# Performance work log

Hardware: AMD Instinct MI355X
Metric: run time of the kernel (lower is better)

Reference implementation:

```python
import jax, jax.numpy as jnp
import numpy as np
from jax import lax

T = 128          # max_length
C_EXPLORE = 10.0 # tanh_exploration
NEG_INF = -1e30  # stand-in for -inf (safe under fp32 softmax)


def setup_inputs() -> dict:
    key = jax.random.key(0)
    ks = jax.random.split(key, 19)
    B, S, E, H = 512, 256, 128, 128
    sc = 0.05
    return {
        "decoder_input": jax.random.normal(ks[0], (B, E), jnp.float32),
        "embedded_inputs": jax.random.normal(ks[1], (S, B, E), jnp.float32),
        "h0": jax.random.normal(ks[2], (B, H), jnp.float32),
        "c0": jax.random.normal(ks[3], (B, H), jnp.float32),
        "context": jax.random.normal(ks[4], (S, B, H), jnp.float32),
        "Wi": jax.random.normal(ks[5], (4 * H, E), jnp.float32) * sc,
        "bi": jax.random.normal(ks[6], (4 * H,), jnp.float32) * sc,
        "Wh": jax.random.normal(ks[7], (4 * H, H), jnp.float32) * sc,
        "bh": jax.random.normal(ks[8], (4 * H,), jnp.float32) * sc,
        "Wq_g": jax.random.normal(ks[9], (H, H), jnp.float32) * sc,
        "bq_g": jax.random.normal(ks[10], (H,), jnp.float32) * sc,
        "Wref_g": jax.random.normal(ks[11], (H, H), jnp.float32) * sc,
        "bref_g": jax.random.normal(ks[12], (H,), jnp.float32) * sc,
        "v_g": jax.random.normal(ks[13], (H,), jnp.float32) * sc,
        "Wq_p": jax.random.normal(ks[14], (H, H), jnp.float32) * sc,
        "bq_p": jax.random.normal(ks[15], (H,), jnp.float32) * sc,
        "Wref_p": jax.random.normal(ks[16], (H, H), jnp.float32) * sc,
        "bref_p": jax.random.normal(ks[17], (H,), jnp.float32) * sc,
        "v_p": jax.random.normal(ks[18], (H,), jnp.float32) * sc,
    }


def _apply_mask(logits, mask, prev_idxs, has_prev):
    # torch: maskk[b, prev]=1; maskk[b,0]=0; logits[maskk]=-inf (only if prev_idxs given)
    B = logits.shape[0]
    m2 = mask.at[jnp.arange(B), prev_idxs].set(True).at[:, 0].set(False)
    m2 = jnp.where(has_prev, m2, mask)
    return jnp.where(m2, NEG_INF, logits), m2


def reference(decoder_input, embedded_inputs, h0, c0, context,
              Wi, bi, Wh, bh,
              Wq_g, bq_g, Wref_g, bref_g, v_g,
              Wq_p, bq_p, Wref_p, bref_p, v_p):
    S, B, E = embedded_inputs.shape
    # conv1d(kernel=1) over fixed context: precompute once (identical math each step)
    e_g = jnp.einsum('oh,sbh->bso', Wref_g, context) + bref_g  # [B,S,H]
    e_p = jnp.einsum('oh,sbh->bso', Wref_p, context) + bref_p  # [B,S,H]
    keys = jax.random.split(jax.random.key(42), T)

    def step(carry, key):
        dec_in, hx, cx, mask, prev, has_prev, finished = carry
        # LSTM cell
        gates = dec_in @ Wi.T + bi + hx @ Wh.T + bh  # [B,4H]
        ig, fg, cg, og = jnp.split(gates, 4, axis=1)
        cy = jax.nn.sigmoid(fg) * cx + jax.nn.sigmoid(ig) * jnp.tanh(cg)
        hy = jax.nn.sigmoid(og) * jnp.tanh(cy)
        # glimpse attention (n_glimpses=1, no tanh clip)
        q = hy @ Wq_g.T + bq_g                                   # [B,H]
        u = jnp.einsum('h,bsh->bs', v_g, jnp.tanh(q[:, None, :] + e_g))
        u, mask = _apply_mask(u, mask, prev, has_prev)
        a = jax.nn.softmax(u, axis=-1)                           # [B,S]
        g_l = jnp.einsum('bsh,bs->bh', e_g, a)                   # bmm(ref, probs)
        # pointer attention with tanh exploration
        q = g_l @ Wq_p.T + bq_p
        u = jnp.einsum('h,bsh->bs', v_p, jnp.tanh(q[:, None, :] + e_p))
        logits = C_EXPLORE * jnp.tanh(u)
        logits, mask = _apply_mask(logits, mask, prev, has_prev)
        probs = jax.nn.softmax(logits, axis=-1)
        # categorical sample from probs == categorical over masked logits
        idx = jax.random.categorical(key, logits).astype(jnp.int32)
        idx = idx * finished
        finished = finished * (idx != 0).astype(jnp.int32)
        dec_in_new = embedded_inputs[idx, jnp.arange(B), :]      # [B,E]
        new_carry = (dec_in_new, hy, cy, mask, idx, jnp.array(True), finished)
        return new_carry, (probs, idx)

    carry0 = (decoder_input, h0, c0,
              jnp.zeros((B, S), bool), jnp.zeros((B,), jnp.int32),
              jnp.array(False), jnp.ones((B,), jnp.int32))
    (_, hx, cx, _, _, _, _), (probs, sels) = lax.scan(step, carry0, keys)
    return probs, sels, hx, cx  # probs [T,B,S], sels [T,B]
```

## Files before the change

kernel.cpp:

```cpp
#include <hip/hip_runtime.h>
#include <stdint.h>

#define BB 512
#define SS 256
#define EE 128
#define HH 128
#define TT 128
#define G4 512

#define NEG_INF_F (-1e30f)
#define TINY_F32  1.17549435e-38f

__device__ __forceinline__ uint32_t rotl32(uint32_t v, int r){ return (v<<r)|(v>>(32-r)); }

__device__ __forceinline__ void threefry2x32(uint32_t k0, uint32_t k1,
                                             uint32_t c0, uint32_t c1,
                                             uint32_t* o0, uint32_t* o1){
  uint32_t ks2 = k0 ^ k1 ^ 0x1BD11BDAu;
  uint32_t x0 = c0 + k0;
  uint32_t x1 = c1 + k1;
#define TF_R(rr) { x0 += x1; x1 = rotl32(x1, rr); x1 ^= x0; }
  TF_R(13) TF_R(15) TF_R(26) TF_R(6)
  x0 += k1; x1 += ks2 + 1u;
  TF_R(17) TF_R(29) TF_R(16) TF_R(24)
  x0 += ks2; x1 += k0 + 2u;
  TF_R(13) TF_R(15) TF_R(26) TF_R(6)
  x0 += k0; x1 += k1 + 3u;
  TF_R(17) TF_R(29) TF_R(16) TF_R(24)
  x0 += k1; x1 += ks2 + 4u;
  TF_R(13) TF_R(15) TF_R(26) TF_R(6)
  x0 += ks2; x1 += k0 + 5u;
#undef TF_R
  *o0 = x0; *o1 = x1;
}

__device__ __forceinline__ float xla_tanhf(float x){
#pragma clang fp contract(off)
  float ax = fabsf(x);
  float xc = fminf(fmaxf(x, -9.0f), 9.0f);
  float x2 = xc*xc;
  float num = -2.76076847742355e-16f;
  num = x2*num + 2.00018790482477e-13f;
  num = x2*num + -8.60467152213735e-11f;
  num = x2*num + 5.12229709037114e-08f;
  num = x2*num + 1.48572235717979e-05f;
  num = x2*num + 6.37261928875436e-04f;
  num = x2*num + 4.89352455891786e-03f;
  num = xc*num;
  float den = 1.19825839466702e-06f;
  den = x2*den + 1.18534705686654e-04f;
  den = x2*den + 2.26843463243900e-03f;
  den = x2*den + 4.89352518554385e-03f;
  return (ax < 4e-4f) ? x : (num/den);
}

__device__ __forceinline__ float xla_sigmoidf(float x){
#pragma clang fp contract(off)
  return 0.5f + 0.5f * xla_tanhf(0.5f * x);
}

__device__ __forceinline__ double wave_sum_f64(double v){
  #pragma unroll
  for (int off = 32; off; off >>= 1) v += __shfl_xor(v, off, 64);
  return v;
}

__global__ __launch_bounds__(256) void precompute_e_kernel(
    const float* __restrict__ ctx, const float* __restrict__ W,
    const float* __restrict__ bias, float* __restrict__ e_out)
{
#pragma clang fp contract(off)
  __shared__ float Ct[64][65];
  __shared__ float Wt[128][65];
  const int tid = threadIdx.x;
  const int tx = tid & 31;
  const int ty = tid >> 5;
  const size_t r0 = (size_t)blockIdx.x * 64;

  double acc[8][4];
  #pragma unroll
  for (int i=0;i<8;++i){
    #pragma unroll
    for (int j=0;j<4;++j) acc[i][j]=0.0;
  }

  for (int kc=0; kc<2; ++kc){
    for (int idx = tid; idx < 64*64; idx += 256){
      const int row = idx >> 6, col = idx & 63;
      Ct[row][col] = ctx[(r0 + row)*HH + kc*64 + col];
    }
    for (int idx = tid; idx < 128*64; idx += 256){
      const int row = idx >> 6, col = idx & 63;
      Wt[row][col] = W[row*HH + kc*64 + col];
    }
    __syncthreads();
    #pragma unroll 4
    for (int kk=0; kk<64; ++kk){
      float cv[8], wv[4];
      #pragma unroll
      for (int i=0;i<8;++i) cv[i] = Ct[ty + 8*i][kk];
      #pragma unroll
      for (int j=0;j<4;++j) wv[j] = Wt[tx + 32*j][kk];
      #pragma unroll
      for (int i=0;i<8;++i){
        #pragma unroll
        for (int j=0;j<4;++j) acc[i][j] += (double)cv[i] * (double)wv[j];
      }
    }
    __syncthreads();
  }
  #pragma unroll
  for (int i=0;i<8;++i){
    const size_t r = r0 + ty + 8*i;
    const int s  = (int)(r >> 9);
    const int bb = (int)(r & 511);
    float* dst = e_out + ((size_t)bb*SS + s)*HH;
    #pragma unroll
    for (int j=0;j<4;++j){
      const int c = tx + 32*j;
      dst[c] = (float)acc[i][j] + bias[c];
    }
  }
}

__global__ void transpose_weights_kernel(
    const float* __restrict__ Wi, const float* __restrict__ Wh,
    const float* __restrict__ Wqg, const float* __restrict__ Wqp,
    float* __restrict__ WiT, float* __restrict__ WhT,
    float* __restrict__ WqgT, float* __restrict__ WqpT)
{
  const int i = blockIdx.x * blockDim.x + threadIdx.x;
  if (i < G4*EE){
    const int j = i / EE, e = i % EE;
    WiT[e*G4 + j] = Wi[i];
    WhT[e*G4 + j] = Wh[i];
  }
  if (i < HH*HH){
    const int o = i / HH, h = i % HH;
    WqgT[h*HH + o] = Wqg[i];
    WqpT[h*HH + o] = Wqp[i];
  }
}

__global__ __launch_bounds__(1024, 4) void decode_kernel(
    const float* __restrict__ dec0, const float* __restrict__ h0v, const float* __restrict__ c0v,
    const float* __restrict__ WiT, const float* __restrict__ WhT,
    const float* __restrict__ bi, const float* __restrict__ bh,
    const float* __restrict__ WqgT, const float* __restrict__ bqg, const float* __restrict__ vg,
    const float* __restrict__ WqpT, const float* __restrict__ bqp, const float* __restrict__ vp,
    const float* __restrict__ e_g, const float* __restrict__ e_p,
    const float* __restrict__ emb,
    float* __restrict__ probs_out, float* __restrict__ sels_out,
    float* __restrict__ hx_out, float* __restrict__ cx_out)
{
#pragma clang fp contract(off)
  const int b = blockIdx.x;
  const int tid = threadIdx.x;
  const int lane = tid & 63;
  const int w = tid >> 6;

  __shared__ float  e_s[SS][HH];
  __shared__ double parts8[8][258];
  __shared__ float  u_s[SS];
  __shared__ float  gates_s[G4];
  __shared__ float  dec_s[EE], hy_s[HH], c_s[HH], gl_s[HH];
  __shared__ float  q4_s[4][132];
  __shared__ float  vg4_s[4][132];
  __shared__ float  vp4_s[4][132];
  __shared__ float  bqg_s[HH], bqp_s[HH];
  __shared__ uint32_t keys0_s[TT], keys1_s[TT];
  __shared__ unsigned char mask_s[SS];
  __shared__ float  fred_s[4];
  __shared__ double dred_s[4];
  __shared__ float  amax_v[4];
  __shared__ int    amax_i[4];
  __shared__ int    idx_sh, fin_sh;

  const float* egb = e_g + (size_t)b*SS*HH;
  const float* epb = e_p + (size_t)b*SS*HH;

  if (tid < HH){
    dec_s[tid] = dec0[b*EE + tid];
    hy_s[tid]  = h0v[b*HH + tid];
    c_s[tid]   = c0v[b*HH + tid];
    const float vgv = vg[tid];
    const float vpv = vp[tid];
    #pragma unroll
    for (int c=0;c<4;++c){ vg4_s[c][tid] = vgv; vp4_s[c][tid] = vpv; }
    bqg_s[tid] = bqg[tid];
    bqp_s[tid] = bqp[tid];
  }
  if (tid < SS) mask_s[tid] = 0;
  if (tid < TT){
    uint32_t kk0, kk1;
    threefry2x32(0u, 42u, 0u, (uint32_t)tid, &kk0, &kk1);
    keys0_s[tid] = kk0; keys1_s[tid] = kk1;
  }
  if (tid == 0) fin_sh = 1;
  for (int idx = tid; idx < SS*32; idx += 1024){
    const int r  = idx >> 5;
    const int c4 = (idx & 31) << 2;
    *(float4*)&e_s[r][c4] = ((const float4*)egb)[idx];
  }
  __syncthreads();

  const int sD = tid >> 2;
  const int q4r = tid & 3;
  float eD[32], eG[32];
  #pragma unroll
  for (int i=0;i<32;++i) eD[i] = e_s[sD][q4r*32 + i];
  {
    const float4* epr = (const float4*)(epb + sD*HH + q4r*32);
    #pragma unroll
    for (int k=0;k<8;++k) *(float4*)&eG[4*k] = epr[k];
  }

  for (int t = 0; t < TT; ++t){
    double* aux = &parts8[0][0];
    double a0 = 0.0;
    if (tid < 512){
      const int j = tid;
      double p0=0.0,p1=0.0,p2=0.0,p3=0.0;
      #pragma unroll 4
      for (int e=0;e<EE;e+=4){
        p0 += (double)dec_s[e+0] * (double)WiT[(e+0)*G4 + j];
        p1 += (double)dec_s[e+1] * (double)WiT[(e+1)*G4 + j];
        p2 += (double)dec_s[e+2] * (double)WiT[(e+2)*G4 + j];
        p3 += (double)dec_s[e+3] * (double)WiT[(e+3)*G4 + j];
      }
      a0 = ((p0+p1)+p2)+p3;
    } else {
      const int j = tid - 512;
      double r0=0.0,r1=0.0,r2=0.0,r3=0.0;
      #pragma unroll 4
      for (int k=0;k<HH;k+=4){
        r0 += (double)hy_s[k+0] * (double)WhT[(k+0)*G4 + j];
        r1 += (double)hy_s[k+1] * (double)WhT[(k+1)*G4 + j];
        r2 += (double)hy_s[k+2] * (double)WhT[(k+2)*G4 + j];
        r3 += (double)hy_s[k+3] * (double)WhT[(k+3)*G4 + j];
      }
      aux[j] = ((r0+r1)+r2)+r3;
    }
    __syncthreads();
    if (tid < 512){
      const int j = tid;
      const float g = (float)a0 + bi[j] + (float)aux[j] + bh[j];
      gates_s[j] = ((j >> 7) == 2) ? xla_tanhf(g) : xla_sigmoidf(g);
    }
    __syncthreads();

    if (tid < HH){
      const int h = tid;
      const float cn = gates_s[HH+h]*c_s[h] + gates_s[h]*gates_s[2*HH+h];
      const float hn = gates_s[3*HH+h]*xla_tanhf(cn);
      c_s[h] = cn; hy_s[h] = hn;
    }
    __syncthreads();

    if (tid < 512){
      const int o = tid & 127, qc = tid >> 7;
      const float* Wc = WqgT + o;
      double acc = 0.0;
      #pragma unroll 8
      for (int i=0;i<32;++i){ const int k = qc*32 + i; acc += (double)hy_s[k] * (double)Wc[(size_t)k*HH]; }
      parts8[qc][o] = acc;
    }
    __syncthreads();
    if (tid < HH){
      const float qq = (float)(((parts8[0][tid]+parts8[1][tid])+parts8[2][tid])+parts8[3][tid]) + bqg_s[tid];
      #pragma unroll
      for (int c=0;c<4;++c) q4_s[c][tid] = qq;
    }
    __syncthreads();

    const bool skipRow = (mask_s[sD] != 0);
    if (!skipRow){
      #pragma unroll
      for (int cc=0; cc<2; ++cc){
        const int hb = q4r*32 + cc*16;
        double acc = 0.0;
        #pragma unroll
        for (int i=0;i<16;++i){
          acc += (double)vg4_s[q4r][hb+i] * (double)xla_tanhf(q4_s[q4r][hb+i] + eD[cc*16+i]);
        }
        parts8[q4r*2 + cc][sD] = acc;
      }
    }
    __syncthreads();

    if (tid < SS){
      float uf;
      if (mask_s[tid]) uf = NEG_INF_F;
      else {
        double u = 0.0;
        #pragma unroll
        for (int wi=0;wi<8;++wi) u += parts8[wi][tid];
        uf = (float)u;
      }
      u_s[tid] = uf;
    }
    __syncthreads();

    {
      float x = 0.0f;
      if (tid < SS){
        x = u_s[tid];
        float wm = x;
        #pragma unroll
        for (int off=32; off; off>>=1) wm = fmaxf(wm, __shfl_xor(wm, off, 64));
        if (lane == 0) fred_s[w] = wm;
      }
      __syncthreads();
      const float m = fmaxf(fmaxf(fred_s[0], fred_s[1]), fmaxf(fred_s[2], fred_s[3]));
      float p = 0.0f;
      if (tid < SS){
        p = mask_s[tid] ? 0.0f : expf(x - m);
        const double zs = wave_sum_f64((double)p);
        if (lane == 0) dred_s[w] = zs;
      }
      __syncthreads();
      const float Z = (float)(dred_s[0] + dred_s[1] + dred_s[2] + dred_s[3]);
      if (tid < SS) u_s[tid] = p / Z;
    }
    __syncthreads();

    {
      const int h = tid & 127, p8 = tid >> 7;
      double acc = 0.0;
      #pragma unroll 8
      for (int sl=0; sl<32; ++sl){
        const int s = p8*32 + sl;
        acc += (double)u_s[s] * (double)e_s[s][h];
      }
      parts8[p8][h] = acc;
    }
    __syncthreads();
    if (tid < HH){
      double g = parts8[0][tid];
      #pragma unroll
      for (int p8=1;p8<8;++p8) g += parts8[p8][tid];
      gl_s[tid] = (float)g;
    }
    __syncthreads();

    if (tid < 512){
      const int o = tid & 127, qc = tid >> 7;
      const float* Wc = WqpT + o;
      double acc = 0.0;
      #pragma unroll 8
      for (int i=0;i<32;++i){ const int k = qc*32 + i; acc += (double)gl_s[k] * (double)Wc[(size_t)k*HH]; }
      parts8[qc][o] = acc;
    }
    __syncthreads();
    if (tid < HH){
      const float qq = (float)(((parts8[0][tid]+parts8[1][tid])+parts8[2][tid])+parts8[3][tid]) + bqp_s[tid];
      #pragma unroll
      for (int c=0;c<4;++c) q4_s[c][tid] = qq;
    }
    __syncthreads();

    if (!skipRow){
      #pragma unroll
      for (int cc=0; cc<2; ++cc){
        const int hb = q4r*32 + cc*16;
        double acc = 0.0;
        #pragma unroll
        for (int i=0;i<16;++i){
          acc += (double)vp4_s[q4r][hb+i] * (double)xla_tanhf(q4_s[q4r][hb+i] + eG[cc*16+i]);
        }
        parts8[q4r*2 + cc][sD] = acc;
      }
    }
    __syncthreads();

    float logit_x = NEG_INF_F;
    if (tid < SS){
      if (!mask_s[tid]){
        double u = 0.0;
        #pragma unroll
        for (int wi=0;wi<8;++wi) u += parts8[wi][tid];
        logit_x = 10.0f * xla_tanhf((float)u);
      }
    }

    {
      const float x = logit_x;
      if (tid < SS){
        float wm = x;
        #pragma unroll
        for (int off=32; off; off>>=1) wm = fmaxf(wm, __shfl_xor(wm, off, 64));
        if (lane == 0) fred_s[w] = wm;
      }
      __syncthreads();
      const float m = fmaxf(fmaxf(fred_s[0], fred_s[1]), fmaxf(fred_s[2], fred_s[3]));
      float p = 0.0f;
      if (tid < SS){
        p = mask_s[tid] ? 0.0f : expf(x - m);
        const double zs = wave_sum_f64((double)p);
        if (lane == 0) dred_s[w] = zs;
      }
      __syncthreads();
      const float Z = (float)(dred_s[0] + dred_s[1] + dred_s[2] + dred_s[3]);
      if (tid < SS) probs_out[((size_t)t*BB + b)*SS + tid] = p / Z;
    }

    {
      if (tid < SS){
        float y = -3.0e38f;
        if (!mask_s[tid]){
          uint32_t r0, r1;
          threefry2x32(keys0_s[t], keys1_s[t], 0u, (uint32_t)(b*SS + tid), &r0, &r1);
          const uint32_t bits = r0 ^ r1;
          const float f = __uint_as_float((bits >> 9) | 0x3f800000u) - 1.0f;
          const float u01 = fmaxf(TINY_F32, f);
          const float g = -logf(-logf(u01));
          y = logit_x + g;
        }
        int bi_ = tid;
        #pragma unroll
        for (int off=32; off; off>>=1){
          const float oy = __shfl_xor(y, off, 64);
          const int oi = __shfl_xor(bi_, off, 64);
          if (oy > y || (oy == y && oi < bi_)){ y = oy; bi_ = oi; }
        }
        if (lane == 0){ amax_v[w] = y; amax_i[w] = bi_; }
      }
      __syncthreads();
      if (tid == 0){
        float bv = amax_v[0]; int bidx = amax_i[0];
        #pragma unroll
        for (int k=1;k<4;++k){
          if (amax_v[k] > bv || (amax_v[k] == bv && amax_i[k] < bidx)){ bv = amax_v[k]; bidx = amax_i[k]; }
        }
        const int fin = fin_sh;
        const int idx = fin ? bidx : 0;
        sels_out[(size_t)t*BB + b] = (float)idx;
        fin_sh = (fin && idx != 0) ? 1 : 0;
        mask_s[idx] = 1;
        mask_s[0] = 0;
        idx_sh = idx;
      }
      __syncthreads();
      if (tid < EE){
        dec_s[tid] = emb[((size_t)idx_sh*BB + b)*EE + tid];
      }
    }
    __syncthreads();
  }

  if (tid < HH){
    hx_out[b*HH + tid] = hy_s[tid];
    cx_out[b*HH + tid] = c_s[tid];
  }
}

__global__ void ws_fail_kernel(float* sels_out){
  if (threadIdx.x == 0 && blockIdx.x == 0) sels_out[0] = -77777.0f;
}

extern "C" void kernel_launch(void* const* d_in, const int* in_sizes, int n_in,
                              void* d_out, int out_size, void* d_ws, size_t ws_size,
                              hipStream_t stream)
{
  const float* decoder_input = (const float*)d_in[0];
  const float* embedded      = (const float*)d_in[1];
  const float* h0            = (const float*)d_in[2];
  const float* c0            = (const float*)d_in[3];
  const float* context       = (const float*)d_in[4];
  const float* Wi            = (const float*)d_in[5];
  const float* bi            = (const float*)d_in[6];
  const float* Wh            = (const float*)d_in[7];
  const float* bh            = (const float*)d_in[8];
  const float* Wq_g          = (const float*)d_in[9];
  const float* bq_g          = (const float*)d_in[10];
  const float* Wref_g        = (const float*)d_in[11];
  const float* bref_g        = (const float*)d_in[12];
  const float* v_g           = (const float*)d_in[13];
  const float* Wq_p          = (const float*)d_in[14];
  const float* bq_p          = (const float*)d_in[15];
  const float* Wref_p        = (const float*)d_in[16];
  const float* bref_p        = (const float*)d_in[17];
  const float* v_p           = (const float*)d_in[18];

  char* ws = (char*)d_ws;
  size_t off = 0;
  auto alloc = [&](size_t bytes) -> void* {
    void* p = ws + off;
    off += (bytes + 255) & ~(size_t)255;
    return p;
  };
  float* e_g   = (float*)alloc((size_t)BB*SS*HH*4);
  float* e_p   = (float*)alloc((size_t)BB*SS*HH*4);
  float* WiT   = (float*)alloc((size_t)EE*G4*4);
  float* WhT   = (float*)alloc((size_t)HH*G4*4);
  float* WqgT  = (float*)alloc((size_t)HH*HH*4);
  float* WqpT  = (float*)alloc((size_t)HH*HH*4);

  float* probs_out = (float*)d_out;
  float* sels_out  = probs_out + (size_t)TT*BB*SS;
  float* hx_out    = sels_out + (size_t)TT*BB;
  float* cx_out    = hx_out + (size_t)BB*HH;

  if (off > ws_size){
    ws_fail_kernel<<<1, 64, 0, stream>>>(sels_out);
    return;
  }

  transpose_weights_kernel<<<(G4*EE + 255)/256, 256, 0, stream>>>(
      Wi, Wh, Wq_g, Wq_p, WiT, WhT, WqgT, WqpT);
  precompute_e_kernel<<<(SS*BB)/64, 256, 0, stream>>>(context, Wref_g, bref_g, e_g);
  precompute_e_kernel<<<(SS*BB)/64, 256, 0, stream>>>(context, Wref_p, bref_p, e_p);

  decode_kernel<<<BB, 1024, 0, stream>>>(
      decoder_input, h0, c0,
      WiT, WhT, bi, bh,
      WqgT, bq_g, v_g,
      WqpT, bq_p, v_p,
      e_g, e_p, embedded,
      probs_out, sels_out, hx_out, cx_out);
}
```

Before: 9.887 ms.

## Stream e_g/e_p from global each step instead of caching in LDS and registers

Drops the 128KB shared-memory copy of e_g and the 64 per-thread registers holding e_g/e_p slices. Both are now re-read from global memory (float4 loads, 8 at a time) inside every timestep, and the glimpse reduction reads e_g from global too. Launch bounds go from 4 to 8 waves per SIMD and the bi/bh biases are cached in LDS. The aim is lower LDS and register pressure so more blocks fit per CU, at the cost of 128 steps of repeated global/L2 traffic over a 256KB-per-batch working set.

Result: slower. 10.33 ms (+4.5%).

```diff
diff --git a/kernel.cpp b/kernel.cpp
--- a/kernel.cpp
+++ b/kernel.cpp
@@ -142,7 +142,7 @@
   }
 }
 
-__global__ __launch_bounds__(1024, 4) void decode_kernel(
+__global__ __launch_bounds__(1024, 8) void decode_kernel(
     const float* __restrict__ dec0, const float* __restrict__ h0v, const float* __restrict__ c0v,
     const float* __restrict__ WiT, const float* __restrict__ WhT,
     const float* __restrict__ bi, const float* __restrict__ bh,
@@ -159,10 +159,10 @@
   const int lane = tid & 63;
   const int w = tid >> 6;
 
-  __shared__ float  e_s[SS][HH];
   __shared__ double parts8[8][258];
   __shared__ float  u_s[SS];
   __shared__ float  gates_s[G4];
+  __shared__ float  bi_s[G4], bh_s[G4];
   __shared__ float  dec_s[EE], hy_s[HH], c_s[HH], gl_s[HH];
   __shared__ float  q4_s[4][132];
   __shared__ float  vg4_s[4][132];
@@ -190,6 +190,7 @@
     bqg_s[tid] = bqg[tid];
     bqp_s[tid] = bqp[tid];
   }
+  if (tid < 512){ bi_s[tid] = bi[tid]; bh_s[tid] = bh[tid]; }
   if (tid < SS) mask_s[tid] = 0;
   if (tid < TT){
     uint32_t kk0, kk1;
@@ -197,23 +198,15 @@
     keys0_s[tid] = kk0; keys1_s[tid] = kk1;
   }
   if (tid == 0) fin_sh = 1;
-  for (int idx = tid; idx < SS*32; idx += 1024){
-    const int r  = idx >> 5;
-    const int c4 = (idx & 31) << 2;
-    *(float4*)&e_s[r][c4] = ((const float4*)egb)[idx];
-  }
   __syncthreads();
 
   const int sD = tid >> 2;
   const int q4r = tid & 3;
-  float eD[32], eG[32];
-  #pragma unroll
-  for (int i=0;i<32;++i) eD[i] = e_s[sD][q4r*32 + i];
-  {
-    const float4* epr = (const float4*)(epb + sD*HH + q4r*32);
-    #pragma unroll
-    for (int k=0;k<8;++k) *(float4*)&eG[4*k] = epr[k];
-  }
+  const float4* eDp = (const float4*)(egb + sD*HH + q4r*32);
+  const float4* eGp = (const float4*)(epb + sD*HH + q4r*32);
+  const int hE  = tid & 127;
+  const int p8E = tid >> 7;
+  const float* eEp = egb + (size_t)p8E*32*HH + hE;
 
   for (int t = 0; t < TT; ++t){
     double* aux = &parts8[0][0];
@@ -244,7 +237,7 @@
     __syncthreads();
     if (tid < 512){
       const int j = tid;
-      const float g = (float)a0 + bi[j] + (float)aux[j] + bh[j];
+      const float g = (float)a0 + bi_s[j] + (float)aux[j] + bh_s[j];
       gates_s[j] = ((j >> 7) == 2) ? xla_tanhf(g) : xla_sigmoidf(g);
     }
     __syncthreads();
@@ -279,9 +272,21 @@
       for (int cc=0; cc<2; ++cc){
         const int hb = q4r*32 + cc*16;
         double acc = 0.0;
-        #pragma unroll
-        for (int i=0;i<16;++i){
-          acc += (double)vg4_s[q4r][hb+i] * (double)xla_tanhf(q4_s[q4r][hb+i] + eD[cc*16+i]);
+        {
+          float ev[8];
+          *(float4*)&ev[0] = eDp[cc*4 + 0];
+          *(float4*)&ev[4] = eDp[cc*4 + 1];
+          #pragma unroll
+          for (int i=0;i<8;++i)
+            acc += (double)vg4_s[q4r][hb+i] * (double)xla_tanhf(q4_s[q4r][hb+i] + ev[i]);
+        }
+        {
+          float ev[8];
+          *(float4*)&ev[0] = eDp[cc*4 + 2];
+          *(float4*)&ev[4] = eDp[cc*4 + 3];
+          #pragma unroll
+          for (int i=0;i<8;++i)
+            acc += (double)vg4_s[q4r][hb+8+i] * (double)xla_tanhf(q4_s[q4r][hb+8+i] + ev[i]);
         }
         parts8[q4r*2 + cc][sD] = acc;
       }
@@ -325,14 +330,12 @@
     __syncthreads();
 
     {
-      const int h = tid & 127, p8 = tid >> 7;
       double acc = 0.0;
       #pragma unroll 8
       for (int sl=0; sl<32; ++sl){
-        const int s = p8*32 + sl;
-        acc += (double)u_s[s] * (double)e_s[s][h];
-      }
-      parts8[p8][h] = acc;
+        acc += (double)u_s[p8E*32 + sl] * (double)eEp[(size_t)sl*HH];
+      }
+      parts8[p8E][hE] = acc;
     }
     __syncthreads();
     if (tid < HH){
@@ -364,9 +367,21 @@
       for (int cc=0; cc<2; ++cc){
         const int hb = q4r*32 + cc*16;
         double acc = 0.0;
-        #pragma unroll
-        for (int i=0;i<16;++i){
-          acc += (double)vp4_s[q4r][hb+i] * (double)xla_tanhf(q4_s[q4r][hb+i] + eG[cc*16+i]);
+        {
+          float ev[8];
+          *(float4*)&ev[0] = eGp[cc*4 + 0];
+          *(float4*)&ev[4] = eGp[cc*4 + 1];
+          #pragma unroll
+          for (int i=0;i<8;++i)
+            acc += (double)vp4_s[q4r][hb+i] * (double)xla_tanhf(q4_s[q4r][hb+i] + ev[i]);
+        }
+        {
+          float ev[8];
+          *(float4*)&ev[0] = eGp[cc*4 + 2];
+          *(float4*)&ev[4] = eGp[cc*4 + 3];
+          #pragma unroll
+          for (int i=0;i<8;++i)
+            acc += (double)vp4_s[q4r][hb+8+i] * (double)xla_tanhf(q4_s[q4r][hb+8+i] + ev[i]);
         }
         parts8[q4r*2 + cc][sD] = acc;
       }
```

## Pack weights for float4 loads and pair tanh evaluations with packed float2 math

Applied to the files above, without the earlier changes.

Re-packs the transposed LSTM and query weights so that each thread reads four consecutive reduction elements as one float4, and uses float4 shared-memory reads for the activation vectors in the gate, query and glimpse reductions. The attention tanh loops now evaluate the rational tanh on two-element float vectors, which can map to packed fp32 instructions. The intent is fewer load instructions and higher ALU throughput in the per-step serial decode loop. Summation order and fp64 accumulation are kept, and contract(off) is still set, so results should match the previous code.

After: 9.975 ms. Within noise of the previous version (+0.9%).

```diff
diff --git a/kernel.cpp b/kernel.cpp
--- a/kernel.cpp
+++ b/kernel.cpp
@@ -10,6 +10,8 @@
 
 #define NEG_INF_F (-1e30f)
 #define TINY_F32  1.17549435e-38f
+
+typedef float v2f __attribute__((ext_vector_type(2)));
 
 __device__ __forceinline__ uint32_t rotl32(uint32_t v, int r){ return (v<<r)|(v>>(32-r)); }
 
@@ -59,6 +61,47 @@
   return 0.5f + 0.5f * xla_tanhf(0.5f * x);
 }
 
+__device__ __forceinline__ v2f splat2(float c){ v2f r; r.x = c; r.y = c; return r; }
+
+__device__ __forceinline__ v2f xla_tanh2(v2f x){
+#pragma clang fp contract(off)
+  v2f xc;
+  xc.x = fminf(fmaxf(x.x, -9.0f), 9.0f);
+  xc.y = fminf(fmaxf(x.y, -9.0f), 9.0f);
+  v2f x2 = xc*xc;
+  v2f num = splat2(-2.76076847742355e-16f);
+  num = x2*num + splat2( 2.00018790482477e-13f);
+  num = x2*num + splat2(-8.60467152213735e-11f);
+  num = x2*num + splat2( 5.12229709037114e-08f);
+  num = x2*num + splat2( 1.48572235717979e-05f);
+  num = x2*num + splat2( 6.37261928875436e-04f);
+  num = x2*num + splat2( 4.89352455891786e-03f);
+  num = xc*num;
+  v2f den = splat2( 1.19825839466702e-06f);
+  den = x2*den + splat2( 1.18534705686654e-04f);
+  den = x2*den + splat2( 2.26843463243900e-03f);
+  den = x2*den + splat2( 4.89352518554385e-03f);
+  v2f r;
+  r.x = num.x/den.x;
+  r.y = num.y/den.y;
+  r.x = (fabsf(x.x) < 4e-4f) ? x.x : r.x;
+  r.y = (fabsf(x.y) < 4e-4f) ? x.y : r.y;
+  return r;
+}
+
+__device__ __forceinline__ void quad_acc(double& acc, const float4 q, const float4 g,
+                                         float e0, float e1, float e2, float e3){
+#pragma clang fp contract(off)
+  v2f a; a.x = q.x + e0; a.y = q.y + e1;
+  v2f t = xla_tanh2(a);
+  acc += (double)g.x * (double)t.x;
+  acc += (double)g.y * (double)t.y;
+  v2f b; b.x = q.z + e2; b.y = q.w + e3;
+  v2f u = xla_tanh2(b);
+  acc += (double)g.z * (double)u.x;
+  acc += (double)g.w * (double)u.y;
+}
+
 __device__ __forceinline__ double wave_sum_f64(double v){
   #pragma unroll
   for (int off = 32; off; off >>= 1) v += __shfl_xor(v, off, 64);
@@ -123,31 +166,33 @@
   }
 }
 
-__global__ void transpose_weights_kernel(
+__global__ void pack_weights_kernel(
     const float* __restrict__ Wi, const float* __restrict__ Wh,
     const float* __restrict__ Wqg, const float* __restrict__ Wqp,
-    float* __restrict__ WiT, float* __restrict__ WhT,
-    float* __restrict__ WqgT, float* __restrict__ WqpT)
+    float* __restrict__ WiP, float* __restrict__ WhP,
+    float* __restrict__ WqgP, float* __restrict__ WqpP)
 {
   const int i = blockIdx.x * blockDim.x + threadIdx.x;
   if (i < G4*EE){
     const int j = i / EE, e = i % EE;
-    WiT[e*G4 + j] = Wi[i];
-    WhT[e*G4 + j] = Wh[i];
+    const size_t d = ((size_t)(e>>2)*G4 + j)*4 + (e&3);
+    WiP[d] = Wi[i];
+    WhP[d] = Wh[i];
   }
   if (i < HH*HH){
-    const int o = i / HH, h = i % HH;
-    WqgT[h*HH + o] = Wqg[i];
-    WqpT[h*HH + o] = Wqp[i];
+    const int o = i / HH, k = i % HH;
+    const size_t d = ((size_t)(k>>2)*HH + o)*4 + (k&3);
+    WqgP[d] = Wqg[i];
+    WqpP[d] = Wqp[i];
   }
 }
 
 __global__ __launch_bounds__(1024, 4) void decode_kernel(
     const float* __restrict__ dec0, const float* __restrict__ h0v, const float* __restrict__ c0v,
-    const float* __restrict__ WiT, const float* __restrict__ WhT,
+    const float* __restrict__ WiP, const float* __restrict__ WhP,
     const float* __restrict__ bi, const float* __restrict__ bh,
-    const float* __restrict__ WqgT, const float* __restrict__ bqg, const float* __restrict__ vg,
-    const float* __restrict__ WqpT, const float* __restrict__ bqp, const float* __restrict__ vp,
+    const float* __restrict__ WqgP, const float* __restrict__ bqg, const float* __restrict__ vg,
+    const float* __restrict__ WqpP, const float* __restrict__ bqp, const float* __restrict__ vp,
     const float* __restrict__ e_g, const float* __restrict__ e_p,
     const float* __restrict__ emb,
     float* __restrict__ probs_out, float* __restrict__ sels_out,
@@ -219,25 +264,30 @@
     double* aux = &parts8[0][0];
     double a0 = 0.0;
     if (tid < 512){
-      const int j = tid;
+      const float4* Wp = (const float4*)WiP + tid;
       double p0=0.0,p1=0.0,p2=0.0,p3=0.0;
-      #pragma unroll 4
-      for (int e=0;e<EE;e+=4){
-        p0 += (double)dec_s[e+0] * (double)WiT[(e+0)*G4 + j];
-        p1 += (double)dec_s[e+1] * (double)WiT[(e+1)*G4 + j];
-        p2 += (double)dec_s[e+2] * (double)WiT[(e+2)*G4 + j];
-        p3 += (double)dec_s[e+3] * (double)WiT[(e+3)*G4 + j];
+      #pragma unroll 8
+      for (int e4=0;e4<32;++e4){
+        const float4 wv = Wp[(size_t)e4*G4];
+        const float4 dv = *(const float4*)&dec_s[e4*4];
+        p0 += (double)dv.x * (double)wv.x;
+        p1 += (double)dv.y * (double)wv.y;
+        p2 += (double)dv.z * (double)wv.z;
+        p3 += (double)dv.w * (double)wv.w;
       }
       a0 = ((p0+p1)+p2)+p3;
     } else {
       const int j = tid - 512;
+      const float4* Wp = (const float4*)WhP + j;
       double r0=0.0,r1=0.0,r2=0.0,r3=0.0;
-      #pragma unroll 4
-      for (int k=0;k<HH;k+=4){
-        r0 += (double)hy_s[k+0] * (double)WhT[(k+0)*G4 + j];
-        r1 += (double)hy_s[k+1] * (double)WhT[(k+1)*G4 + j];
-        r2 += (double)hy_s[k+2] * (double)WhT[(k+2)*G4 + j];
-        r3 += (double)hy_s[k+3] * (double)WhT[(k+3)*G4 + j];
+      #pragma unroll 8
+      for (int k4=0;k4<32;++k4){
+        const float4 wv = Wp[(size_t)k4*G4];
+        const float4 hv = *(const float4*)&hy_s[k4*4];
+        r0 += (double)hv.x * (double)wv.x;
+        r1 += (double)hv.y * (double)wv.y;
+        r2 += (double)hv.z * (double)wv.z;
+        r3 += (double)hv.w * (double)wv.w;
       }
       aux[j] = ((r0+r1)+r2)+r3;
     }
@@ -259,10 +309,17 @@
 
     if (tid < 512){
       const int o = tid & 127, qc = tid >> 7;
-      const float* Wc = WqgT + o;
+      const float4* Wc = (const float4*)WqgP + (size_t)qc*8*HH + o;
       double acc = 0.0;
-      #pragma unroll 8
-      for (int i=0;i<32;++i){ const int k = qc*32 + i; acc += (double)hy_s[k] * (double)Wc[(size_t)k*HH]; }
+      #pragma unroll
+      for (int i8=0;i8<8;++i8){
+        const float4 wv = Wc[(size_t)i8*HH];
+        const float4 hv = *(const float4*)&hy_s[qc*32 + i8*4];
+        acc += (double)hv.x * (double)wv.x;
+        acc += (double)hv.y * (double)wv.y;
+        acc += (double)hv.z * (double)wv.z;
+        acc += (double)hv.w * (double)wv.w;
+      }
       parts8[qc][o] = acc;
     }
     __syncthreads();
@@ -278,11 +335,20 @@
       #pragma unroll
       for (int cc=0; cc<2; ++cc){
         const int hb = q4r*32 + cc*16;
+        const float4 qa = *(const float4*)&q4_s[q4r][hb+0];
+        const float4 qb = *(const float4*)&q4_s[q4r][hb+4];
+        const float4 qc4= *(const float4*)&q4_s[q4r][hb+8];
+        const float4 qd = *(const float4*)&q4_s[q4r][hb+12];
+        const float4 ga = *(const float4*)&vg4_s[q4r][hb+0];
+        const float4 gb = *(const float4*)&vg4_s[q4r][hb+4];
+        const float4 gc = *(const float4*)&vg4_s[q4r][hb+8];
+        const float4 gd = *(const float4*)&vg4_s[q4r][hb+12];
+        const int eb = cc*16;
         double acc = 0.0;
-        #pragma unroll
-        for (int i=0;i<16;++i){
-          acc += (double)vg4_s[q4r][hb+i] * (double)xla_tanhf(q4_s[q4r][hb+i] + eD[cc*16+i]);
-        }
+        quad_acc(acc, qa, ga, eD[eb+0],  eD[eb+1],  eD[eb+2],  eD[eb+3]);
+        quad_acc(acc, qb, gb, eD[eb+4],  eD[eb+5],  eD[eb+6],  eD[eb+7]);
+        quad_acc(acc, qc4,gc, eD[eb+8],  eD[eb+9],  eD[eb+10], eD[eb+11]);
+        quad_acc(acc, qd, gd, eD[eb+12], eD[eb+13], eD[eb+14], eD[eb+15]);
         parts8[q4r*2 + cc][sD] = acc;
       }
     }
@@ -327,10 +393,14 @@
     {
       const int h = tid & 127, p8 = tid >> 7;
       double acc = 0.0;
-      #pragma unroll 8
-      for (int sl=0; sl<32; ++sl){
-        const int s = p8*32 + sl;
-        acc += (double)u_s[s] * (double)e_s[s][h];
+      #pragma unroll
+      for (int g4i=0; g4i<8; ++g4i){
+        const int s0 = p8*32 + g4i*4;
+        const float4 uv = *(const float4*)&u_s[s0];
+        acc += (double)uv.x * (double)e_s[s0+0][h];
+        acc += (double)uv.y * (double)e_s[s0+1][h];
+        acc += (double)uv.z * (double)e_s[s0+2][h];
+        acc += (double)uv.w * (double)e_s[s0+3][h];
       }
       parts8[p8][h] = acc;
     }
@@ -345,10 +415,17 @@
 
     if (tid < 512){
       const int o = tid & 127, qc = tid >> 7;
-      const float* Wc = WqpT + o;
+      const float4* Wc = (const float4*)WqpP + (size_t)qc*8*HH + o;
       double acc = 0.0;
-      #pragma unroll 8
-      for (int i=0;i<32;++i){ const int k = qc*32 + i; acc += (double)gl_s[k] * (double)Wc[(size_t)k*HH]; }
+      #pragma unroll
+      for (int i8=0;i8<8;++i8){
+        const float4 wv = Wc[(size_t)i8*HH];
+        const float4 hv = *(const float4*)&gl_s[qc*32 + i8*4];
+        acc += (double)hv.x * (double)wv.x;
+        acc += (double)hv.y * (double)wv.y;
+        acc += (double)hv.z * (double)wv.z;
+        acc += (double)hv.w * (double)wv.w;
+      }
       parts8[qc][o] = acc;
     }
     __syncthreads();
@@ -363,11 +440,20 @@
       #pragma unroll
       for (int cc=0; cc<2; ++cc){
         const int hb = q4r*32 + cc*16;
+        const float4 qa = *(const float4*)&q4_s[q4r][hb+0];
+        const float4 qb = *(const float4*)&q4_s[q4r][hb+4];
+        const float4 qc4= *(const float4*)&q4_s[q4r][hb+8];
+        const float4 qd = *(const float4*)&q4_s[q4r][hb+12];
+        const float4 ga = *(const float4*)&vp4_s[q4r][hb+0];
+        const float4 gb = *(const float4*)&vp4_s[q4r][hb+4];
+        const float4 gc = *(const float4*)&vp4_s[q4r][hb+8];
+        const float4 gd = *(const float4*)&vp4_s[q4r][hb+12];
+        const int eb = cc*16;
         double acc = 0.0;
-        #pragma unroll
-        for (int i=0;i<16;++i){
-          acc += (double)vp4_s[q4r][hb+i] * (double)xla_tanhf(q4_s[q4r][hb+i] + eG[cc*16+i]);
-        }
+        quad_acc(acc, qa, ga, eG[eb+0],  eG[eb+1],  eG[eb+2],  eG[eb+3]);
+        quad_acc(acc, qb, gb, eG[eb+4],  eG[eb+5],  eG[eb+6],  eG[eb+7]);
+        quad_acc(acc, qc4,gc, eG[eb+8],  eG[eb+9],  eG[eb+10], eG[eb+11]);
+        quad_acc(acc, qd, gd, eG[eb+12], eG[eb+13], eG[eb+14], eG[eb+15]);
         parts8[q4r*2 + cc][sD] = acc;
       }
     }
@@ -489,12 +575,12 @@
     off += (bytes + 255) & ~(size_t)255;
     return p;
   };
-  float* e_g   = (float*)alloc((size_t)BB*SS*HH*4);
-  float* e_p   = (float*)alloc((size_t)BB*SS*HH*4);
-  float* WiT   = (float*)alloc((size_t)EE*G4*4);
-  float* WhT   = (float*)alloc((size_t)HH*G4*4);
-  float* WqgT  = (float*)alloc((size_t)HH*HH*4);
-  float* WqpT  = (float*)alloc((size_t)HH*HH*4);
+  float* e_g  = (float*)alloc((size_t)BB*SS*HH*4);
+  float* e_p  = (float*)alloc((size_t)BB*SS*HH*4);
+  float* WiP  = (float*)alloc((size_t)EE*G4*4);
+  float* WhP  = (float*)alloc((size_t)HH*G4*4);
+  float* WqgP = (float*)alloc((size_t)HH*HH*4);
+  float* WqpP = (float*)alloc((size_t)HH*HH*4);
 
   float* probs_out = (float*)d_out;
   float* sels_out  = probs_out + (size_t)TT*BB*SS;
@@ -506,16 +592,16 @@
     return;
   }
 
-  transpose_weights_kernel<<<(G4*EE + 255)/256, 256, 0, stream>>>(
-      Wi, Wh, Wq_g, Wq_p, WiT, WhT, WqgT, WqpT);
+  pack_weights_kernel<<<(G4*EE + 255)/256, 256, 0, stream>>>(
+      Wi, Wh, Wq_g, Wq_p, WiP, WhP, WqgP, WqpP);
   precompute_e_kernel<<<(SS*BB)/64, 256, 0, stream>>>(context, Wref_g, bref_g, e_g);
   precompute_e_kernel<<<(SS*BB)/64, 256, 0, stream>>>(context, Wref_p, bref_p, e_p);
 
   decode_kernel<<<BB, 1024, 0, stream>>>(
       decoder_input, h0, c0,
-      WiT, WhT, bi, bh,
-      WqgT, bq_g, v_g,
-      WqpT, bq_p, v_p,
+      WiP, WhP, bi, bh,
+      WqgP, bq_g, v_g,
+      WqpP, bq_p, v_p,
       e_g, e_p, embedded,
       probs_out, sels_out, hx_out, cx_out);
 }
```
